# Kernel optimization log

Hardware: AMD Instinct MI355X
Metric: run time of the kernel (lower is better)

Reference implementation:

```python
import jax, jax.numpy as jnp
import numpy as np

NS = 10000   # servers
ND = 50000   # devices
H = 512      # hidden dim
E = 300000   # edges per relation
L = 4        # total SAGEConv layers (input + 2 hidden + output)


def segment_mean(vals, seg, num_segments):
    # scatter-mean aggregation (PyG 'mean' aggr); empty segments -> 0
    s = jax.ops.segment_sum(vals, seg, num_segments=num_segments)
    cnt = jax.ops.segment_sum(jnp.ones((seg.shape[0], 1), vals.dtype), seg,
                              num_segments=num_segments)
    return s / jnp.maximum(cnt, 1.0)


def setup_inputs() -> dict:
    key = jax.random.key(0)
    ks = jax.random.split(key, 12)
    scale = 0.05
    return {
        "x_servers": jax.random.normal(ks[0], (NS, 64), jnp.float32),
        "x_devices": jax.random.normal(ks[1], (ND, 32), jnp.float32),
        "W_srv": jax.random.normal(ks[2], (64, H), jnp.float32) * scale,
        "b_srv": jnp.zeros((H,), jnp.float32),
        "W_dev": jax.random.normal(ks[3], (32, H), jnp.float32) * scale,
        "b_dev": jnp.zeros((H,), jnp.float32),
        # rel 0: servers->devices (updates devices); rel 1: devices->servers
        "Wl": jax.random.normal(ks[4], (L, 2, H, H), jnp.float32) * scale,
        "bl": jnp.zeros((L, 2, H), jnp.float32),
        "Wr": jax.random.normal(ks[5], (L, 2, H, H), jnp.float32) * scale,
        "e_sd_src": jax.random.randint(ks[6], (E,), 0, NS, jnp.int32),
        "e_sd_dst": jax.random.randint(ks[7], (E,), 0, ND, jnp.int32),
        "e_ds_src": jax.random.randint(ks[8], (E,), 0, ND, jnp.int32),
        "e_ds_dst": jax.random.randint(ks[9], (E,), 0, NS, jnp.int32),
    }


def reference(x_servers, x_devices, W_srv, b_srv, W_dev, b_dev,
              Wl, bl, Wr, e_sd_src, e_sd_dst, e_ds_src, e_ds_dst):
    # per-type input projection (no activation, as in GNN.forward)
    hs = x_servers @ W_srv + b_srv   # [NS, H]
    hd = x_devices @ W_dev + b_dev   # [ND, H]
    for l in range(L):
        # gather source features per edge, scatter-mean to destination
        agg_d = segment_mean(hs[e_sd_src], e_sd_dst, ND)  # servers -> devices
        agg_s = segment_mean(hd[e_ds_src], e_ds_dst, NS)  # devices -> servers
        # SAGEConv: lin_l(agg) + lin_r(x_dst), then relu
        new_d = jax.nn.relu(agg_d @ Wl[l, 0] + bl[l, 0] + hd @ Wr[l, 0])
        new_s = jax.nn.relu(agg_s @ Wl[l, 1] + bl[l, 1] + hs @ Wr[l, 1])
        hs, hd = new_s, new_d
    return (hs, hd)
```

## Files before the change

kernel.cpp:

```cpp
#include <hip/hip_runtime.h>
#include <cstdint>

#define NSRV 10000
#define NDEV 50000
#define HDIM 512
#define NEDGE 300000
#define NLAY 4
#define SCHUNK 2048
#define NCH_D ((NDEV + SCHUNK - 1) / SCHUNK)
#define NCH_S ((NSRV + SCHUNK - 1) / SCHUNK)

typedef unsigned int u32;
typedef unsigned short u16;

typedef __bf16 bf16x8 __attribute__((ext_vector_type(8)));
typedef float f32x4 __attribute__((ext_vector_type(4)));

__device__ __forceinline__ float bflo(u32 u) { return __uint_as_float(u << 16); }
__device__ __forceinline__ float bfhi(u32 u) { return __uint_as_float(u & 0xffff0000u); }
__device__ __forceinline__ float bf2f(u16 v) { return __uint_as_float((u32)v << 16); }
__device__ __forceinline__ u16 f2bf(float f) {
    u32 u = __float_as_uint(f);
    u += 0x7fffu + ((u >> 16) & 1u);
    return (u16)(u >> 16);
}
__device__ __forceinline__ u32 pack2(float a, float b) {
    return (u32)f2bf(a) | ((u32)f2bf(b) << 16);
}
__device__ __forceinline__ u32 relu2(u32 v) {
    return pack2(fmaxf(bflo(v), 0.f), fmaxf(bfhi(v), 0.f));
}
__device__ __forceinline__ u32 addrelu2(u32 v, u32 a) {
    return pack2(fmaxf(bflo(v) + bflo(a), 0.f), fmaxf(bfhi(v) + bfhi(a), 0.f));
}

__global__ void cast_bf16(const float* __restrict__ src, u16* __restrict__ dst, int n2) {
    int i = blockIdx.x * 256 + threadIdx.x;
    if (i < n2) {
        float2 v = *(const float2*)(src + 2 * (size_t)i);
        *(u32*)(dst + 2 * (size_t)i) = pack2(v.x, v.y);
    }
}

__global__ void transpose_w(const float* __restrict__ Wl, const float* __restrict__ Wr,
                            u16* __restrict__ WlT, u16* __restrict__ WrT) {
    __shared__ float t[32][33];
    int z = blockIdx.z;
    const float* Wsrc = ((z < 8) ? Wl : Wr) + (size_t)(z & 7) * HDIM * HDIM;
    u16* Wdst = ((z < 8) ? WlT : WrT) + (size_t)(z & 7) * HDIM * HDIM;
    int n0 = blockIdx.x * 32, k0 = blockIdx.y * 32;
    int x = threadIdx.x, y = threadIdx.y;
#pragma unroll
    for (int i = 0; i < 4; ++i)
        t[y + 8 * i][x] = Wsrc[(size_t)(k0 + y + 8 * i) * HDIM + n0 + x];
    __syncthreads();
    if (x < 16) {
#pragma unroll
        for (int i = 0; i < 4; ++i) {
            int n = n0 + y + 8 * i;
            u32 v = pack2(t[2 * x][y + 8 * i], t[2 * x + 1][y + 8 * i]);
            *(u32*)(Wdst + (size_t)n * HDIM + k0 + 2 * x) = v;
        }
    }
}

template <int K>
__global__ void transpose_wp(const float* __restrict__ W, u16* __restrict__ WT) {
    __shared__ float t[32][33];
    int n0 = blockIdx.x * 32, k0 = blockIdx.y * 32;
    int x = threadIdx.x, y = threadIdx.y;
#pragma unroll
    for (int i = 0; i < 4; ++i)
        t[y + 8 * i][x] = W[(size_t)(k0 + y + 8 * i) * HDIM + n0 + x];
    __syncthreads();
    if (x < 16) {
#pragma unroll
        for (int i = 0; i < 4; ++i) {
            int n = n0 + y + 8 * i;
            u32 v = pack2(t[2 * x][y + 8 * i], t[2 * x + 1][y + 8 * i]);
            *(u32*)(WT + (size_t)n * K + k0 + 2 * x) = v;
        }
    }
}

template <int KTOT>
__launch_bounds__(256, 2)
__global__ void proj_gemm(const u16* __restrict__ A, const u16* __restrict__ B,
                          const float* __restrict__ bias, u16* __restrict__ C, int M) {
    constexpr int NKC = KTOT / 8;
    __shared__ __align__(16) u16 As[NKC][128][8];
    __shared__ __align__(16) u16 Bs[NKC][128][8];
    const int tid = threadIdx.x;
    const int lane = tid & 63;
    const int w = tid >> 6;
    const int m0 = blockIdx.x * 128, n0 = blockIdx.y * 128;
    const int wm = w >> 1, wn = w & 1;
    const int g = lane >> 4, r = lane & 15;

    for (int idx = tid; idx < NKC * 128; idx += 256) {
        int row = idx / NKC, kc = idx % NKC;
        int ra = m0 + row; if (ra > M - 1) ra = M - 1;
        *(uint4*)&As[kc][row][0] = *(const uint4*)(A + (size_t)ra * KTOT + kc * 8);
        *(uint4*)&Bs[kc][row][0] = *(const uint4*)(B + (size_t)(n0 + row) * KTOT + kc * 8);
    }
    __syncthreads();

    f32x4 acc[4][4];
#pragma unroll
    for (int i = 0; i < 4; ++i)
#pragma unroll
        for (int j = 0; j < 4; ++j) acc[i][j] = (f32x4){0.f, 0.f, 0.f, 0.f};

#pragma unroll
    for (int t = 0; t < KTOT / 32; ++t) {
        bf16x8 af[4], bfr[4];
#pragma unroll
        for (int i = 0; i < 4; ++i) {
            af[i]  = *(const bf16x8*)&As[t * 4 + g][wm * 64 + i * 16 + r][0];
            bfr[i] = *(const bf16x8*)&Bs[t * 4 + g][wn * 64 + i * 16 + r][0];
        }
#pragma unroll
        for (int i = 0; i < 4; ++i)
#pragma unroll
            for (int j = 0; j < 4; ++j)
                acc[i][j] = __builtin_amdgcn_mfma_f32_16x16x32_bf16(af[i], bfr[j], acc[i][j], 0, 0, 0);
    }
    __syncthreads();

    float bv[4];
#pragma unroll
    for (int j = 0; j < 4; ++j) bv[j] = bias[n0 + wn * 64 + j * 16 + r];

    u16* ep = ((u16*)As) + w * 1024;
    const int rr = lane >> 3;
    const int cc = (lane & 7) * 8;
#pragma unroll
    for (int i = 0; i < 4; ++i) {
#pragma unroll
        for (int j = 0; j < 4; ++j)
#pragma unroll
            for (int q = 0; q < 4; ++q)
                ep[(g * 4 + q) * 64 + j * 16 + r] = f2bf(acc[i][j][q] + bv[j]);
        __syncthreads();
        int row0 = m0 + wm * 64 + i * 16 + rr;
        int row1 = row0 + 8;
        uint4 v0 = *(uint4*)&ep[rr * 64 + cc];
        uint4 v1 = *(uint4*)&ep[(rr + 8) * 64 + cc];
        if (row0 < M) *(uint4*)(C + (size_t)row0 * HDIM + n0 + wn * 64 + cc) = v0;
        if (row1 < M) *(uint4*)(C + (size_t)row1 * HDIM + n0 + wn * 64 + cc) = v1;
        __syncthreads();
    }
}

__launch_bounds__(256, 2)
__global__ void gemm_plain(const u16* __restrict__ A, const u16* __restrict__ B,
                           u16* __restrict__ C, int M, int MB) {
    const int b = blockIdx.x;
    const int mi = (b >> 5) * 8 + (b & 7);
    const int ni = (b >> 3) & 3;
    if (mi >= MB) return;

    __shared__ __align__(16) u16 As[2][4][128][8];
    __shared__ __align__(16) u16 Bs[2][4][128][8];
    const int tid = threadIdx.x;
    const int lane = tid & 63;
    const int w = tid >> 6;
    const int m0 = mi * 128, n0 = ni * 128;
    const int wm = w >> 1, wn = w & 1;
    const int g = lane >> 4, r = lane & 15;

    const int srow = tid >> 2;
    const int skc  = tid & 3;

    f32x4 acc[4][4];
#pragma unroll
    for (int i = 0; i < 4; ++i)
#pragma unroll
        for (int j = 0; j < 4; ++j) acc[i][j] = (f32x4){0.f, 0.f, 0.f, 0.f};

    uint4 ra0, ra1, rb0, rb1;
    auto gload = [&](int kt) {
        const int kb = kt * 32 + skc * 8;
        int r0 = m0 + srow;      if (r0 > M - 1) r0 = M - 1;
        int r1 = m0 + srow + 64; if (r1 > M - 1) r1 = M - 1;
        ra0 = *(const uint4*)(A + (size_t)r0 * HDIM + kb);
        ra1 = *(const uint4*)(A + (size_t)r1 * HDIM + kb);
        rb0 = *(const uint4*)(B + (size_t)(n0 + srow) * HDIM + kb);
        rb1 = *(const uint4*)(B + (size_t)(n0 + srow + 64) * HDIM + kb);
    };
    auto swrite = [&](int buf) {
        *(uint4*)&As[buf][skc][srow][0]      = ra0;
        *(uint4*)&As[buf][skc][srow + 64][0] = ra1;
        *(uint4*)&Bs[buf][skc][srow][0]      = rb0;
        *(uint4*)&Bs[buf][skc][srow + 64][0] = rb1;
    };
    auto compute = [&](int buf) {
        bf16x8 af[4], bfr[4];
#pragma unroll
        for (int i = 0; i < 4; ++i) {
            af[i]  = *(const bf16x8*)&As[buf][g][wm * 64 + i * 16 + r][0];
            bfr[i] = *(const bf16x8*)&Bs[buf][g][wn * 64 + i * 16 + r][0];
        }
#pragma unroll
        for (int i = 0; i < 4; ++i)
#pragma unroll
            for (int j = 0; j < 4; ++j)
                acc[i][j] = __builtin_amdgcn_mfma_f32_16x16x32_bf16(af[i], bfr[j], acc[i][j], 0, 0, 0);
    };

    gload(0);
    swrite(0);
    __syncthreads();
    for (int kt = 0; kt < 16; ++kt) {
        if (kt < 15) gload(kt + 1);
        compute(kt & 1);
        if (kt < 15) swrite((kt + 1) & 1);
        __syncthreads();
    }

    u16* ep = ((u16*)As) + w * 1024;
    const int rr = lane >> 3;
    const int cc = (lane & 7) * 8;
#pragma unroll
    for (int i = 0; i < 4; ++i) {
#pragma unroll
        for (int j = 0; j < 4; ++j)
#pragma unroll
            for (int q = 0; q < 4; ++q)
                ep[(g * 4 + q) * 64 + j * 16 + r] = f2bf(acc[i][j][q]);
        __syncthreads();
        int row0 = m0 + wm * 64 + i * 16 + rr;
        int row1 = row0 + 8;
        uint4 v0 = *(uint4*)&ep[rr * 64 + cc];
        uint4 v1 = *(uint4*)&ep[(rr + 8) * 64 + cc];
        if (row0 < M) *(uint4*)(C + (size_t)row0 * HDIM + n0 + wn * 64 + cc) = v0;
        if (row1 < M) *(uint4*)(C + (size_t)row1 * HDIM + n0 + wn * 64 + cc) = v1;
        __syncthreads();
    }
}

__global__ void count_k(const int* __restrict__ d_sd, const int* __restrict__ d_ds,
                        int* __restrict__ cd, int* __restrict__ cs) {
    int i = blockIdx.x * 256 + threadIdx.x;
    if (i < NEDGE) atomicAdd(&cd[d_sd[i]], 1);
    else if (i < 2 * NEDGE) atomicAdd(&cs[d_ds[i - NEDGE]], 1);
}

__global__ void scan_a_both(const int* __restrict__ cd, int* __restrict__ od, int* __restrict__ csd,
                            const int* __restrict__ cs, int* __restrict__ os, int* __restrict__ css) {
    __shared__ int wsum[4];
    int blk = blockIdx.x;
    const int* c; int* o; int* csum; int n; int cb;
    if (blk < NCH_D) { c = cd; o = od; csum = csd; n = NDEV; cb = blk; }
    else             { c = cs; o = os; csum = css; n = NSRV; cb = blk - NCH_D; }
    int tid = threadIdx.x;
    int base = cb * SCHUNK;
    int idx0 = base + tid * 8;
    int v[8];
    int s = 0;
#pragma unroll
    for (int i = 0; i < 8; ++i) {
        int idx = idx0 + i;
        v[i] = (idx < n) ? c[idx] : 0;
        s += v[i];
    }
    int lane = tid & 63, wv = tid >> 6;
    int ss = s;
#pragma unroll
    for (int off = 1; off < 64; off <<= 1) {
        int t = __shfl_up(ss, off);
        if (lane >= off) ss += t;
    }
    if (lane == 63) wsum[wv] = ss;
    __syncthreads();
    int woff = 0;
#pragma unroll
    for (int i = 0; i < 4; ++i)
        if (i < wv) woff += wsum[i];
    int ex = woff + ss - s;
#pragma unroll
    for (int i = 0; i < 8; ++i) {
        int idx = idx0 + i;
        if (idx < n) o[idx] = ex;
        ex += v[i];
    }
    if (tid == 255) csum[cb] = woff + ss;
}

__global__ void scan_k(const int* __restrict__ cA, int* __restrict__ oA, int* __restrict__ uA, int nA,
                       const int* __restrict__ cB, int* __restrict__ oB, int* __restrict__ uB, int nB) {
    const int* c; int* o; int* u; int n;
    if (blockIdx.x == 0) { c = cA; o = oA; u = uA; n = nA; }
    else                 { c = cB; o = oB; u = uB; n = nB; }
    int lane = threadIdx.x;
    int carry = 0;
    for (int base = 0; base < n; base += 64) {
        int idx = base + lane;
        int v = (idx < n) ? c[idx] : 0;
        int s = v;
#pragma unroll
        for (int off = 1; off < 64; off <<= 1) {
            int t = __shfl_up(s, off);
            if (lane >= off) s += t;
        }
        if (idx < n) { int ex = carry + s - v; o[idx] = ex; u[idx] = ex; }
        carry += __shfl(s, 63);
    }
}

__global__ void scan_c_both(int* __restrict__ od, int* __restrict__ curd, const int* __restrict__ csxd,
                            int* __restrict__ os, int* __restrict__ curs, const int* __restrict__ csxs) {
    int i = blockIdx.x * 256 + threadIdx.x;
    if (i < NDEV) {
        int v = od[i] + csxd[i / SCHUNK];
        od[i] = v;
        curd[i] = v;
    } else if (i < NDEV + NSRV) {
        int j = i - NDEV;
        int v = os[j] + csxs[j / SCHUNK];
        os[j] = v;
        curs[j] = v;
    }
}

__global__ void fill_k(const int* __restrict__ s_sd, const int* __restrict__ d_sd,
                       int* __restrict__ cur_d, int* __restrict__ srcs_d,
                       const int* __restrict__ s_ds, const int* __restrict__ d_ds,
                       int* __restrict__ cur_s, int* __restrict__ srcs_s) {
    int i = blockIdx.x * 256 + threadIdx.x;
    if (i < NEDGE) {
        int p = atomicAdd(&cur_d[d_sd[i]], 1);
        srcs_d[p] = s_sd[i];
    } else if (i < 2 * NEDGE) {
        int j = i - NEDGE;
        int p = atomicAdd(&cur_s[d_ds[j]], 1);
        srcs_s[p] = s_ds[j];
    }
}

__global__ void aggregate_both(const u16* __restrict__ ps, const u16* __restrict__ hd,
                               const int* __restrict__ offs_d, const int* __restrict__ cnt_d,
                               const int* __restrict__ src_d,
                               const int* __restrict__ offs_s, const int* __restrict__ cnt_s,
                               const int* __restrict__ src_s,
                               u16* __restrict__ agg_d, u16* __restrict__ agg_s) {
    int wv = threadIdx.x >> 6, lane = threadIdx.x & 63;
    int d = blockIdx.x * 4 + wv;
    const u16* h; const int* offs; const int* cnt; const int* srcs; u16* agg; int idx;
    if (d < NDEV)              { h = ps; offs = offs_d; cnt = cnt_d; srcs = src_d; agg = agg_d; idx = d; }
    else if (d < NDEV + NSRV)  { h = hd; offs = offs_s; cnt = cnt_s; srcs = src_s; agg = agg_s; idx = d - NDEV; }
    else return;
    int beg = offs[idx], deg = cnt[idx];
    float acc[8] = {0.f, 0.f, 0.f, 0.f, 0.f, 0.f, 0.f, 0.f};
    const size_t lanecol = (size_t)lane * 8;
    auto accum = [&](const uint4& q) {
        acc[0] += bflo(q.x); acc[1] += bfhi(q.x);
        acc[2] += bflo(q.y); acc[3] += bfhi(q.y);
        acc[4] += bflo(q.z); acc[5] += bfhi(q.z);
        acc[6] += bflo(q.w); acc[7] += bfhi(q.w);
    };
    for (int t0 = 0; t0 < deg; t0 += 64) {
        int nch = min(64, deg - t0);
        int sv = (t0 + lane < deg) ? srcs[beg + t0 + lane] : 0;
        int j = 0;
        for (; j + 8 <= nch; j += 8) {
            uint4 q[8];
#pragma unroll
            for (int u_ = 0; u_ < 8; ++u_) {
                int s = __shfl(sv, j + u_);
                q[u_] = *(const uint4*)(h + (size_t)s * HDIM + lanecol);
            }
#pragma unroll
            for (int u_ = 0; u_ < 8; ++u_) accum(q[u_]);
        }
        for (; j + 4 <= nch; j += 4) {
            uint4 q[4];
#pragma unroll
            for (int u_ = 0; u_ < 4; ++u_) {
                int s = __shfl(sv, j + u_);
                q[u_] = *(const uint4*)(h + (size_t)s * HDIM + lanecol);
            }
#pragma unroll
            for (int u_ = 0; u_ < 4; ++u_) accum(q[u_]);
        }
        for (; j < nch; ++j) {
            int s = __shfl(sv, j);
            const uint4 q = *(const uint4*)(h + (size_t)s * HDIM + lanecol);
            accum(q);
        }
    }
    float sc = 1.f / (float)(deg > 0 ? deg : 1);
    uint4 o;
    o.x = pack2(acc[0] * sc, acc[1] * sc);
    o.y = pack2(acc[2] * sc, acc[3] * sc);
    o.z = pack2(acc[4] * sc, acc[5] * sc);
    o.w = pack2(acc[6] * sc, acc[7] * sc);
    *(uint4*)(agg + (size_t)idx * HDIM + lanecol) = o;
}

__launch_bounds__(512, 2)
__global__ void gemm_both(const u16* __restrict__ A1d, const u16* __restrict__ A2d,
                          const u16* __restrict__ B1d, const u16* __restrict__ B2d,
                          const u16* __restrict__ AGGd, const float* __restrict__ bd,
                          u16* __restrict__ Cd, int Md, int MBd, int GD,
                          const u16* __restrict__ A1s, const u16* __restrict__ A2s,
                          const u16* __restrict__ B1s, const u16* __restrict__ B2s,
                          const float* __restrict__ bs, u16* __restrict__ Cs, int Ms, int MBs) {
    int b = blockIdx.x;
    const u16 *A1, *A2, *B1, *B2, *AGG; const float* bias; u16* C; int M, MB, kt0;
    if (b < GD) {
        A1 = A1d; A2 = A2d; B1 = B1d; B2 = B2d; AGG = AGGd;
        bias = bd; C = Cd; M = Md; MB = MBd; kt0 = 16;
    } else {
        b -= GD;
        A1 = A1s; A2 = A2s; B1 = B1s; B2 = B2s; AGG = nullptr;
        bias = bs; C = Cs; M = Ms; MB = MBs; kt0 = 0;
    }
    const int mi = (b >> 5) * 8 + (b & 7);
    const int ni = (b >> 3) & 3;
    if (mi >= MB) return;

    __shared__ __align__(16) u16 As[2][4][256][8];
    __shared__ __align__(16) u16 Bs[2][4][128][8];
    const int tid = threadIdx.x;
    const int lane = tid & 63;
    const int w = tid >> 6;
    const int m0 = mi * 256, n0 = ni * 128;
    const int wm = w >> 1, wn = w & 1;
    const int g = lane >> 4, r = lane & 15;

    const int srow = tid >> 2;
    const int skc  = tid & 3;

    f32x4 acc[4][4];
#pragma unroll
    for (int i = 0; i < 4; ++i)
#pragma unroll
        for (int j = 0; j < 4; ++j) acc[i][j] = (f32x4){0.f, 0.f, 0.f, 0.f};

    uint4 ra0, ra1, rb0;
    auto gload = [&](int kt) {
        const u16* Ap = (kt < 16) ? A1 : A2;
        const u16* Bp = (kt < 16) ? B1 : B2;
        const int kb = (kt & 15) * 32 + skc * 8;
        int r0 = m0 + srow;       if (r0 > M - 1) r0 = M - 1;
        int r1 = m0 + srow + 128; if (r1 > M - 1) r1 = M - 1;
        ra0 = *(const uint4*)(Ap + (size_t)r0 * HDIM + kb);
        ra1 = *(const uint4*)(Ap + (size_t)r1 * HDIM + kb);
        rb0 = *(const uint4*)(Bp + (size_t)(n0 + srow) * HDIM + kb);
    };
    auto swrite = [&](int buf) {
        *(uint4*)&As[buf][skc][srow][0]       = ra0;
        *(uint4*)&As[buf][skc][srow + 128][0] = ra1;
        *(uint4*)&Bs[buf][skc][srow][0]       = rb0;
    };
    auto compute = [&](int buf) {
        bf16x8 af[4], bfr[4];
#pragma unroll
        for (int i = 0; i < 4; ++i) {
            af[i]  = *(const bf16x8*)&As[buf][g][wm * 64 + i * 16 + r][0];
            bfr[i] = *(const bf16x8*)&Bs[buf][g][wn * 64 + i * 16 + r][0];
        }
#pragma unroll
        for (int i = 0; i < 4; ++i)
#pragma unroll
            for (int j = 0; j < 4; ++j)
                acc[i][j] = __builtin_amdgcn_mfma_f32_16x16x32_bf16(af[i], bfr[j], acc[i][j], 0, 0, 0);
    };

    gload(kt0);
    swrite(0);
    __syncthreads();
    for (int kt = kt0; kt < 32; ++kt) {
        if (kt < 31) gload(kt + 1);
        compute(kt & 1);
        if (kt < 31) swrite((kt + 1) & 1);
        __syncthreads();
    }

    float bv[4];
#pragma unroll
    for (int j = 0; j < 4; ++j) bv[j] = bias[n0 + wn * 64 + j * 16 + r];

    u16* ep = ((u16*)As) + w * 2048;
    const int rr = lane >> 3;
    const int cc = (lane & 7) * 8;
#pragma unroll
    for (int ih = 0; ih < 2; ++ih) {
#pragma unroll
        for (int ii = 0; ii < 2; ++ii) {
            int i = ih * 2 + ii;
#pragma unroll
            for (int j = 0; j < 4; ++j)
#pragma unroll
                for (int q = 0; q < 4; ++q)
                    ep[ii * 1024 + (g * 4 + q) * 64 + j * 16 + r] =
                        f2bf(acc[i][j][q] + bv[j]);
        }
        __syncthreads();
#pragma unroll
        for (int ii = 0; ii < 2; ++ii) {
            int i = ih * 2 + ii;
            int row0 = m0 + wm * 64 + i * 16 + rr;
            int row1 = row0 + 8;
            uint4 v0 = *(uint4*)&ep[ii * 1024 + rr * 64 + cc];
            uint4 v1 = *(uint4*)&ep[ii * 1024 + (rr + 8) * 64 + cc];
            size_t c0 = (size_t)row0 * HDIM + n0 + wn * 64 + cc;
            size_t c1 = (size_t)row1 * HDIM + n0 + wn * 64 + cc;
            if (row0 < M) {
                uint4 o;
                if (AGG) {
                    uint4 a = *(const uint4*)(AGG + c0);
                    o.x = addrelu2(v0.x, a.x); o.y = addrelu2(v0.y, a.y);
                    o.z = addrelu2(v0.z, a.z); o.w = addrelu2(v0.w, a.w);
                } else {
                    o.x = relu2(v0.x); o.y = relu2(v0.y);
                    o.z = relu2(v0.z); o.w = relu2(v0.w);
                }
                *(uint4*)(C + c0) = o;
            }
            if (row1 < M) {
                uint4 o;
                if (AGG) {
                    uint4 a = *(const uint4*)(AGG + c1);
                    o.x = addrelu2(v1.x, a.x); o.y = addrelu2(v1.y, a.y);
                    o.z = addrelu2(v1.z, a.z); o.w = addrelu2(v1.w, a.w);
                } else {
                    o.x = relu2(v1.x); o.y = relu2(v1.y);
                    o.z = relu2(v1.z); o.w = relu2(v1.w);
                }
                *(uint4*)(C + c1) = o;
            }
        }
        __syncthreads();
    }
}

__global__ void expand_k(float* out, int lo, int hi) {
    const u16* src = (const u16*)out;
    int j = lo + blockIdx.x * 256 + threadIdx.x;
    if (j < hi) {
        float v = bf2f(src[j]);
        out[(size_t)j] = v;
    }
}
__global__ void expand_final(float* out, int n) {
    __shared__ u16 tmp[4096];
    const u16* src = (const u16*)out;
    int tid = threadIdx.x;
    for (int i = tid; i < n; i += blockDim.x) tmp[i] = src[i];
    __syncthreads();
    for (int i = tid; i < n; i += blockDim.x) out[(size_t)i] = bf2f(tmp[i]);
}

extern "C" void kernel_launch(void* const* d_in, const int* in_sizes, int n_in,
                              void* d_out, int out_size, void* d_ws, size_t ws_size,
                              hipStream_t stream) {
    const float* x_s   = (const float*)d_in[0];
    const float* x_d   = (const float*)d_in[1];
    const float* W_srv = (const float*)d_in[2];
    const float* b_srv = (const float*)d_in[3];
    const float* W_dev = (const float*)d_in[4];
    const float* b_dev = (const float*)d_in[5];
    const float* Wl    = (const float*)d_in[6];
    const float* bl    = (const float*)d_in[7];
    const float* Wr    = (const float*)d_in[8];
    const int* e_sd_src = (const int*)d_in[9];
    const int* e_sd_dst = (const int*)d_in[10];
    const int* e_ds_src = (const int*)d_in[11];
    const int* e_ds_dst = (const int*)d_in[12];

    const size_t NTOT = (size_t)(NSRV + NDEV) * HDIM;
    float* fout = (float*)d_out;
    u16* u = (u16*)d_out;
    u16* hA_s = u;
    u16* hA_d = u + (size_t)NSRV * HDIM;
    u16* hB_s = u + NTOT;
    u16* hB_d = u + NTOT + (size_t)NSRV * HDIM;

    char* p = (char*)d_ws;
    auto carve = [&](size_t bytes) -> void* {
        void* ret = (void*)p;
        p += (bytes + 255) & ~(size_t)255;
        return ret;
    };
    int* cnt_d = (int*)carve((size_t)NDEV * 4);
    int* cnt_s = (int*)carve((size_t)NSRV * 4);
    int* off_d = (int*)carve((size_t)NDEV * 4);
    int* off_s = (int*)carve((size_t)NSRV * 4);
    int* cur_d = (int*)carve((size_t)NDEV * 4);
    int* cur_s = (int*)carve((size_t)NSRV * 4);
    int* src_d = (int*)carve((size_t)NEDGE * 4);
    int* src_s = (int*)carve((size_t)NEDGE * 4);
    int* csum_d = (int*)carve(64 * 4);
    int* csum_s = (int*)carve(64 * 4);
    int* csx_d  = (int*)carve(64 * 4);
    int* csx_s  = (int*)carve(64 * 4);
    u16* WlT   = (u16*)carve((size_t)NLAY * 2 * HDIM * HDIM * 2);
    u16* WrT   = (u16*)carve((size_t)NLAY * 2 * HDIM * HDIM * 2);
    u16* agg_d = (u16*)carve((size_t)NDEV * HDIM * 2);
    u16* agg_s = (u16*)carve((size_t)NSRV * HDIM * 2);
    u16* ps    = (u16*)carve((size_t)NSRV * HDIM * 2);
    u16* xb_s  = (u16*)carve((size_t)NSRV * 64 * 2);
    u16* xb_d  = (u16*)carve((size_t)NDEV * 32 * 2);
    u16* WTp_s = (u16*)carve((size_t)HDIM * 64 * 2);
    u16* WTp_d = (u16*)carve((size_t)HDIM * 32 * 2);

    hipMemsetAsync(cnt_d, 0, (size_t)NDEV * 4, stream);
    hipMemsetAsync(cnt_s, 0, (size_t)NSRV * 4, stream);

    cast_bf16<<<(NSRV * 64 / 2 + 255) / 256, 256, 0, stream>>>(x_s, xb_s, NSRV * 64 / 2);
    cast_bf16<<<(NDEV * 32 / 2 + 255) / 256, 256, 0, stream>>>(x_d, xb_d, NDEV * 32 / 2);
    transpose_wp<64><<<dim3(16, 2), dim3(32, 8), 0, stream>>>(W_srv, WTp_s);
    transpose_wp<32><<<dim3(16, 1), dim3(32, 8), 0, stream>>>(W_dev, WTp_d);
    transpose_w<<<dim3(16, 16, 16), dim3(32, 8), 0, stream>>>(Wl, Wr, WlT, WrT);

    proj_gemm<64><<<dim3((NSRV + 127) / 128, 4), 256, 0, stream>>>(xb_s, WTp_s, b_srv, hA_s, NSRV);
    proj_gemm<32><<<dim3((NDEV + 127) / 128, 4), 256, 0, stream>>>(xb_d, WTp_d, b_dev, hA_d, NDEV);

    count_k<<<(2 * NEDGE + 255) / 256, 256, 0, stream>>>(e_sd_dst, e_ds_dst, cnt_d, cnt_s);
    scan_a_both<<<NCH_D + NCH_S, 256, 0, stream>>>(cnt_d, off_d, csum_d, cnt_s, off_s, csum_s);
    scan_k<<<2, 64, 0, stream>>>(csum_d, csx_d, csx_d, NCH_D, csum_s, csx_s, csx_s, NCH_S);
    scan_c_both<<<(NDEV + NSRV + 255) / 256, 256, 0, stream>>>(off_d, cur_d, csx_d, off_s, cur_s, csx_s);
    fill_k<<<(2 * NEDGE + 255) / 256, 256, 0, stream>>>(e_sd_src, e_sd_dst, cur_d, src_d,
                                                        e_ds_src, e_ds_dst, cur_s, src_s);

    const int MB_D = (NDEV + 255) / 256;
    const int MB_S = (NSRV + 255) / 256;
    const int GD = ((MB_D + 7) / 8) * 32;
    const int GS = ((MB_S + 7) / 8) * 32;
    const int MB_P = (NSRV + 127) / 128;
    const int GP = ((MB_P + 7) / 8) * 32;

    for (int l = 0; l < NLAY; ++l) {
        const u16* hs_in = (l & 1) ? hB_s : hA_s;
        const u16* hd_in = (l & 1) ? hB_d : hA_d;
        u16* hs_out = (l & 1) ? hA_s : hB_s;
        u16* hd_out = (l & 1) ? hA_d : hB_d;

        const u16* WlT0 = WlT + (size_t)(l * 2 + 0) * HDIM * HDIM;
        const u16* WrT0 = WrT + (size_t)(l * 2 + 0) * HDIM * HDIM;
        const u16* WlT1 = WlT + (size_t)(l * 2 + 1) * HDIM * HDIM;
        const u16* WrT1 = WrT + (size_t)(l * 2 + 1) * HDIM * HDIM;
        const float* bl0 = bl + (size_t)(l * 2 + 0) * HDIM;
        const float* bl1 = bl + (size_t)(l * 2 + 1) * HDIM;

        gemm_plain<<<GP, 256, 0, stream>>>(hs_in, WlT0, ps, NSRV, MB_P);
        aggregate_both<<<(NDEV + NSRV + 3) / 4, 256, 0, stream>>>(
            ps, hd_in, off_d, cnt_d, src_d, off_s, cnt_s, src_s, agg_d, agg_s);
        gemm_both<<<GD + GS, 512, 0, stream>>>(
            hd_in, hd_in, WrT0, WrT0, agg_d, bl0, hd_out, NDEV, MB_D, GD,
            agg_s, hs_in, WlT1, WrT1, bl1, hs_out, NSRV, MB_S);
    }

    int hi = (int)NTOT;
    while (hi > 4000 && (hi % 2 == 0)) {
        int lo = hi / 2;
        int nblk = (hi - lo + 255) / 256;
        expand_k<<<nblk, 256, 0, stream>>>(fout, lo, hi);
        hi = lo;
    }
    expand_final<<<1, 512, 0, stream>>>(fout, hi);
}
```

Baseline: 837.1 us.

## Fuse device-side mean aggregation into GEMM epilogue, drop agg_d buffer

The servers-to-devices mean aggregation of the pre-projected server features (ps) moves out of the separate aggregate kernel and into the device GEMM epilogue. Each thread gathers neighbor rows for its 8 output columns, averages them, adds the result to the GEMM output and applies relu. This removes the write and re-read of a 50000x512 bf16 agg_d buffer and part of a kernel launch. In exchange the gather runs serially per row inside the GEMM epilogue with little memory-level parallelism, which may stall GEMM blocks and hurt occupancy.

```diff
diff --git a/kernel.cpp b/kernel.cpp
--- a/kernel.cpp
+++ b/kernel.cpp
@@ -29,9 +29,6 @@
 }
 __device__ __forceinline__ u32 relu2(u32 v) {
     return pack2(fmaxf(bflo(v), 0.f), fmaxf(bfhi(v), 0.f));
-}
-__device__ __forceinline__ u32 addrelu2(u32 v, u32 a) {
-    return pack2(fmaxf(bflo(v) + bflo(a), 0.f), fmaxf(bfhi(v) + bfhi(a), 0.f));
 }
 
 __global__ void cast_bf16(const float* __restrict__ src, u16* __restrict__ dst, int n2) {
@@ -338,19 +335,13 @@
     }
 }
 
-__global__ void aggregate_both(const u16* __restrict__ ps, const u16* __restrict__ hd,
-                               const int* __restrict__ offs_d, const int* __restrict__ cnt_d,
-                               const int* __restrict__ src_d,
-                               const int* __restrict__ offs_s, const int* __restrict__ cnt_s,
-                               const int* __restrict__ src_s,
-                               u16* __restrict__ agg_d, u16* __restrict__ agg_s) {
+__global__ void aggregate_srv(const u16* __restrict__ hd,
+                              const int* __restrict__ offs_s, const int* __restrict__ cnt_s,
+                              const int* __restrict__ src_s, u16* __restrict__ agg_s) {
     int wv = threadIdx.x >> 6, lane = threadIdx.x & 63;
-    int d = blockIdx.x * 4 + wv;
-    const u16* h; const int* offs; const int* cnt; const int* srcs; u16* agg; int idx;
-    if (d < NDEV)              { h = ps; offs = offs_d; cnt = cnt_d; srcs = src_d; agg = agg_d; idx = d; }
-    else if (d < NDEV + NSRV)  { h = hd; offs = offs_s; cnt = cnt_s; srcs = src_s; agg = agg_s; idx = d - NDEV; }
-    else return;
-    int beg = offs[idx], deg = cnt[idx];
+    int idx = blockIdx.x * 4 + wv;
+    if (idx >= NSRV) return;
+    int beg = offs_s[idx], deg = cnt_s[idx];
     float acc[8] = {0.f, 0.f, 0.f, 0.f, 0.f, 0.f, 0.f, 0.f};
     const size_t lanecol = (size_t)lane * 8;
     auto accum = [&](const uint4& q) {
@@ -361,14 +352,14 @@
     };
     for (int t0 = 0; t0 < deg; t0 += 64) {
         int nch = min(64, deg - t0);
-        int sv = (t0 + lane < deg) ? srcs[beg + t0 + lane] : 0;
+        int sv = (t0 + lane < deg) ? src_s[beg + t0 + lane] : 0;
         int j = 0;
         for (; j + 8 <= nch; j += 8) {
             uint4 q[8];
 #pragma unroll
             for (int u_ = 0; u_ < 8; ++u_) {
                 int s = __shfl(sv, j + u_);
-                q[u_] = *(const uint4*)(h + (size_t)s * HDIM + lanecol);
+                q[u_] = *(const uint4*)(hd + (size_t)s * HDIM + lanecol);
             }
 #pragma unroll
             for (int u_ = 0; u_ < 8; ++u_) accum(q[u_]);
@@ -378,43 +369,45 @@
 #pragma unroll
             for (int u_ = 0; u_ < 4; ++u_) {
                 int s = __shfl(sv, j + u_);
-                q[u_] = *(const uint4*)(h + (size_t)s * HDIM + lanecol);
+                q[u_] = *(const uint4*)(hd + (size_t)s * HDIM + lanecol);
             }
 #pragma unroll
             for (int u_ = 0; u_ < 4; ++u_) accum(q[u_]);
         }
         for (; j < nch; ++j) {
             int s = __shfl(sv, j);
-            const uint4 q = *(const uint4*)(h + (size_t)s * HDIM + lanecol);
+            const uint4 q = *(const uint4*)(hd + (size_t)s * HDIM + lanecol);
             accum(q);
         }
     }
-    float sc = 1.f / (float)(deg > 0 ? deg : 1);
+    float sc = (deg > 0) ? 1.f / (float)deg : 1.f;
     uint4 o;
     o.x = pack2(acc[0] * sc, acc[1] * sc);
     o.y = pack2(acc[2] * sc, acc[3] * sc);
     o.z = pack2(acc[4] * sc, acc[5] * sc);
     o.w = pack2(acc[6] * sc, acc[7] * sc);
-    *(uint4*)(agg + (size_t)idx * HDIM + lanecol) = o;
+    *(uint4*)(agg_s + (size_t)idx * HDIM + lanecol) = o;
 }
 
 __launch_bounds__(512, 2)
-__global__ void gemm_both(const u16* __restrict__ A1d, const u16* __restrict__ A2d,
-                          const u16* __restrict__ B1d, const u16* __restrict__ B2d,
-                          const u16* __restrict__ AGGd, const float* __restrict__ bd,
-                          u16* __restrict__ Cd, int Md, int MBd, int GD,
+__global__ void gemm_both(const u16* __restrict__ A2d, const u16* __restrict__ B2d,
+                          const u16* __restrict__ PSp, const int* __restrict__ offs_d,
+                          const int* __restrict__ cnt_d, const int* __restrict__ src_d,
+                          const float* __restrict__ bd, u16* __restrict__ Cd,
+                          int Md, int MBd, int GD,
                           const u16* __restrict__ A1s, const u16* __restrict__ A2s,
                           const u16* __restrict__ B1s, const u16* __restrict__ B2s,
                           const float* __restrict__ bs, u16* __restrict__ Cs, int Ms, int MBs) {
     int b = blockIdx.x;
-    const u16 *A1, *A2, *B1, *B2, *AGG; const float* bias; u16* C; int M, MB, kt0;
+    const u16 *A1, *A2, *B1, *B2; const float* bias; u16* C; int M, MB, kt0;
+    bool isdev;
     if (b < GD) {
-        A1 = A1d; A2 = A2d; B1 = B1d; B2 = B2d; AGG = AGGd;
-        bias = bd; C = Cd; M = Md; MB = MBd; kt0 = 16;
+        A1 = A2d; A2 = A2d; B1 = B2d; B2 = B2d;
+        bias = bd; C = Cd; M = Md; MB = MBd; kt0 = 16; isdev = true;
     } else {
         b -= GD;
-        A1 = A1s; A2 = A2s; B1 = B1s; B2 = B2s; AGG = nullptr;
-        bias = bs; C = Cs; M = Ms; MB = MBs; kt0 = 0;
+        A1 = A1s; A2 = A2s; B1 = B1s; B2 = B2s;
+        bias = bs; C = Cs; M = Ms; MB = MBs; kt0 = 0; isdev = false;
     }
     const int mi = (b >> 5) * 8 + (b & 7);
     const int ni = (b >> 3) & 3;
@@ -485,6 +478,35 @@
     u16* ep = ((u16*)As) + w * 2048;
     const int rr = lane >> 3;
     const int cc = (lane & 7) * 8;
+    const int colbase = n0 + wn * 64 + cc;
+
+    auto finish_row = [&](int row, uint4 v) {
+        size_t coff = (size_t)row * HDIM + colbase;
+        uint4 o;
+        if (isdev) {
+            int beg = offs_d[row], deg = cnt_d[row];
+            float a0 = 0.f, a1 = 0.f, a2 = 0.f, a3 = 0.f,
+                  a4 = 0.f, a5 = 0.f, a6 = 0.f, a7 = 0.f;
+            for (int j = 0; j < deg; ++j) {
+                int s = src_d[beg + j];
+                uint4 q = *(const uint4*)(PSp + (size_t)s * HDIM + colbase);
+                a0 += bflo(q.x); a1 += bfhi(q.x);
+                a2 += bflo(q.y); a3 += bfhi(q.y);
+                a4 += bflo(q.z); a5 += bfhi(q.z);
+                a6 += bflo(q.w); a7 += bfhi(q.w);
+            }
+            float sc = (deg > 0) ? 1.f / (float)deg : 1.f;
+            o.x = pack2(fmaxf(bflo(v.x) + a0 * sc, 0.f), fmaxf(bfhi(v.x) + a1 * sc, 0.f));
+            o.y = pack2(fmaxf(bflo(v.y) + a2 * sc, 0.f), fmaxf(bfhi(v.y) + a3 * sc, 0.f));
+            o.z = pack2(fmaxf(bflo(v.z) + a4 * sc, 0.f), fmaxf(bfhi(v.z) + a5 * sc, 0.f));
+            o.w = pack2(fmaxf(bflo(v.w) + a6 * sc, 0.f), fmaxf(bfhi(v.w) + a7 * sc, 0.f));
+        } else {
+            o.x = relu2(v.x); o.y = relu2(v.y);
+            o.z = relu2(v.z); o.w = relu2(v.w);
+        }
+        *(uint4*)(C + coff) = o;
+    };
+
 #pragma unroll
     for (int ih = 0; ih < 2; ++ih) {
 #pragma unroll
@@ -505,32 +527,8 @@
             int row1 = row0 + 8;
             uint4 v0 = *(uint4*)&ep[ii * 1024 + rr * 64 + cc];
             uint4 v1 = *(uint4*)&ep[ii * 1024 + (rr + 8) * 64 + cc];
-            size_t c0 = (size_t)row0 * HDIM + n0 + wn * 64 + cc;
-            size_t c1 = (size_t)row1 * HDIM + n0 + wn * 64 + cc;
-            if (row0 < M) {
-                uint4 o;
-                if (AGG) {
-                    uint4 a = *(const uint4*)(AGG + c0);
-                    o.x = addrelu2(v0.x, a.x); o.y = addrelu2(v0.y, a.y);
-                    o.z = addrelu2(v0.z, a.z); o.w = addrelu2(v0.w, a.w);
-                } else {
-                    o.x = relu2(v0.x); o.y = relu2(v0.y);
-                    o.z = relu2(v0.z); o.w = relu2(v0.w);
-                }
-                *(uint4*)(C + c0) = o;
-            }
-            if (row1 < M) {
-                uint4 o;
-                if (AGG) {
-                    uint4 a = *(const uint4*)(AGG + c1);
-                    o.x = addrelu2(v1.x, a.x); o.y = addrelu2(v1.y, a.y);
-                    o.z = addrelu2(v1.z, a.z); o.w = addrelu2(v1.w, a.w);
-                } else {
-                    o.x = relu2(v1.x); o.y = relu2(v1.y);
-                    o.z = relu2(v1.z); o.w = relu2(v1.w);
-                }
-                *(uint4*)(C + c1) = o;
-            }
+            if (row0 < M) finish_row(row0, v0);
+            if (row1 < M) finish_row(row1, v1);
         }
         __syncthreads();
     }
@@ -598,7 +596,6 @@
     int* csx_s  = (int*)carve(64 * 4);
     u16* WlT   = (u16*)carve((size_t)NLAY * 2 * HDIM * HDIM * 2);
     u16* WrT   = (u16*)carve((size_t)NLAY * 2 * HDIM * HDIM * 2);
-    u16* agg_d = (u16*)carve((size_t)NDEV * HDIM * 2);
     u16* agg_s = (u16*)carve((size_t)NSRV * HDIM * 2);
     u16* ps    = (u16*)carve((size_t)NSRV * HDIM * 2);
     u16* xb_s  = (u16*)carve((size_t)NSRV * 64 * 2);
@@ -646,10 +643,9 @@
         const float* bl1 = bl + (size_t)(l * 2 + 1) * HDIM;
 
         gemm_plain<<<GP, 256, 0, stream>>>(hs_in, WlT0, ps, NSRV, MB_P);
-        aggregate_both<<<(NDEV + NSRV + 3) / 4, 256, 0, stream>>>(
-            ps, hd_in, off_d, cnt_d, src_d, off_s, cnt_s, src_s, agg_d, agg_s);
+        aggregate_srv<<<(NSRV + 3) / 4, 256, 0, stream>>>(hd_in, off_s, cnt_s, src_s, agg_s);
         gemm_both<<<GD + GS, 512, 0, stream>>>(
-            hd_in, hd_in, WrT0, WrT0, agg_d, bl0, hd_out, NDEV, MB_D, GD,
+            hd_in, WrT0, ps, off_d, cnt_d, src_d, bl0, hd_out, NDEV, MB_D, GD,
             agg_s, hs_in, WlT1, WrT1, bl1, hs_out, NSRV, MB_S);
     }
 
```

Result: slower. 1.086 ms (+29.8%).
